# Optimization experiments

Measured on AMD Instinct MI355X. Metric: run time of the kernel, lower is better.

Reference implementation:

```python
import jax, jax.numpy as jnp
import numpy as np

VOCAB = 14
EMBED = 10
HIDDEN = 50
MLP = 50
PAD_IDX = 0
BATCH = 4096
SEQ = 2048


def setup_inputs() -> dict:
    key = jax.random.key(0)
    ks = jax.random.split(key, 10)
    tokens = jax.random.randint(ks[0], (BATCH, SEQ), 0, VOCAB, dtype=jnp.int64 if jax.config.jax_enable_x64 else jnp.int32)
    s_lstm = 1.0 / np.sqrt(HIDDEN)
    s_mlp1 = 1.0 / np.sqrt(HIDDEN)
    s_mlp2 = 1.0 / np.sqrt(MLP)
    emb = jax.random.normal(ks[1], (VOCAB, EMBED), jnp.float32)
    emb = emb.at[PAD_IDX].set(0.0)  # padding_idx row is zero in torch Embedding
    W_ih = jax.random.uniform(ks[2], (4 * HIDDEN, EMBED), jnp.float32, -s_lstm, s_lstm)
    W_hh = jax.random.uniform(ks[3], (4 * HIDDEN, HIDDEN), jnp.float32, -s_lstm, s_lstm)
    b_ih = jax.random.uniform(ks[4], (4 * HIDDEN,), jnp.float32, -s_lstm, s_lstm)
    b_hh = jax.random.uniform(ks[5], (4 * HIDDEN,), jnp.float32, -s_lstm, s_lstm)
    W1 = jax.random.uniform(ks[6], (MLP, HIDDEN), jnp.float32, -s_mlp1, s_mlp1)
    b1 = jax.random.uniform(ks[7], (MLP,), jnp.float32, -s_mlp1, s_mlp1)
    W2 = jax.random.uniform(ks[8], (1, MLP), jnp.float32, -s_mlp2, s_mlp2)
    b2 = jax.random.uniform(ks[9], (1,), jnp.float32, -s_mlp2, s_mlp2)
    return {"input": tokens, "emb": emb, "W_ih": W_ih, "W_hh": W_hh,
            "b_ih": b_ih, "b_hh": b_hh, "W1": W1, "b1": b1, "W2": W2, "b2": b2}


def reference(input, emb, W_ih, W_hh, b_ih, b_hh, W1, b1, W2, b2):
    x = emb[input]                                   # [B, T, E]
    mask = (input != PAD_IDX).astype(emb.dtype)      # [B, T]
    xs = jnp.swapaxes(x, 0, 1)                       # [T, B, E]
    ms = jnp.swapaxes(mask, 0, 1)[:, :, None]        # [T, B, 1]
    B = input.shape[0]

    def step(carry, inp):
        h, c = carry
        xt, mt = inp
        gates = xt @ W_ih.T + b_ih + h @ W_hh.T + b_hh  # [B, 4H], order i,f,g,o
        i, f, g, o = jnp.split(gates, 4, axis=-1)
        i = jax.nn.sigmoid(i)
        f = jax.nn.sigmoid(f)
        g = jnp.tanh(g)
        o = jax.nn.sigmoid(o)
        c_new = f * c + i * g
        h_new = o * jnp.tanh(c_new)
        # blend: keep old state on padded positions
        h = h_new * mt + h * (1.0 - mt)
        c = c_new * mt + c * (1.0 - mt)
        return (h, c), None

    h0 = jnp.zeros((B, HIDDEN), emb.dtype)
    c0 = jnp.zeros((B, HIDDEN), emb.dtype)
    (h, c), _ = jax.lax.scan(step, (h0, c0), (xs, ms))
    hidden = h @ W1.T + b1                            # [B, MLP]
    out = jax.nn.sigmoid(hidden @ W2.T + b2)          # [B, 1]
    return out
```

## Files before the change

kernel.cpp:

```cpp
#include <hip/hip_runtime.h>

#define BATCH 4096
#define SEQ   2048
#define EMB   10
#define HID   50
#define VOCAB 14
#define TROW  2052

using bf16x8 = __attribute__((ext_vector_type(8))) short;
using f32x4  = __attribute__((ext_vector_type(4))) float;

__device__ __forceinline__ short f2bf(float f) {
  unsigned u = __builtin_bit_cast(unsigned, f);
  u = (u + 0x7FFFu + ((u >> 16) & 1u)) >> 16;
  return (short)u;
}
__device__ __forceinline__ unsigned f2bf2(float lo, float hi) {
  return (unsigned)(unsigned short)f2bf(lo) | ((unsigned)(unsigned short)f2bf(hi) << 16);
}
__device__ __forceinline__ float fsigm(float x) {
  return __builtin_amdgcn_rcpf(1.0f + __builtin_amdgcn_exp2f(x * -1.44269504f));
}

__global__ void prep_kernel(const float* __restrict__ emb,  const float* __restrict__ W_ih,
                            const float* __restrict__ W_hh, const float* __restrict__ b_ih,
                            const float* __restrict__ b_hh, short* __restrict__ Apack) {
  int idx = blockIdx.x * 256 + threadIdx.x;
  if (idx >= 13 * 2 * 64 * 8) return;
  int j    = idx & 7;
  int lane = (idx >> 3) & 63;
  int kf   = (idx >> 9) & 1;
  int tid  = idx >> 10;
  int m    = lane & 15;
  int q    = m >> 2, g = m & 3;
  int jh   = (tid < 10) ? (2 * ((tid >> 1) * 4 + q) + (tid & 1))
                        : (40 + (tid - 10) * 4 + q);
  int k    = kf * 32 + (lane >> 4) * 8 + j;
  float v = 0.0f;
  if (jh < HID) {
    int R = g * HID + jh;
    float scale = (g == 2) ? -2.885390082f : -1.442695041f;
    if (k < HID) {
      v = W_hh[R * HID + k] * scale;
    } else {
      int vo = k - HID;
      float s = b_ih[R] + b_hh[R];
      for (int e = 0; e < EMB; ++e) s += emb[vo * EMB + e] * W_ih[R * EMB + e];
      v = s * scale;
    }
  }
  Apack[idx] = f2bf(v);
}

__global__ __launch_bounds__(512, 1) void lstm_kernel(
    const int* __restrict__ tokens, const short* __restrict__ Apack,
    const float* __restrict__ W1, const float* __restrict__ b1,
    const float* __restrict__ W2, const float* __restrict__ b2,
    float* __restrict__ out) {
  __shared__ __align__(16) unsigned char toku8[16 * TROW];
  __shared__ __align__(16) short hbuf[2][16 * 64];
  __shared__ float hfin[16 * 52];
  __shared__ float mlp_hid[16 * 52];

  const int tid  = threadIdx.x;
  const int lane = tid & 63;
  const int wv   = tid >> 6;
  const int b0   = blockIdx.x * 16;
  const int bB   = lane & 15;
  const int jj   = lane >> 4;

  const bool two = (0xA7 >> wv) & 1;
  const int  fr  = __builtin_popcount(0xA7 & ((1 << wv) - 1));
  const int  sr  = __builtin_popcount(0x58 & ((1 << wv) - 1));
  const int  p   = fr * 4 + jj;
  const int  jhS = 40 + sr * 4 + jj;
  const bool sval = !two && (jhS < HID);

  const int t0 = two ? (fr * 2) : (10 + sr);
  bf16x8 Af00 = *(const bf16x8*)(Apack + ((t0 * 2 + 0) * 64 + lane) * 8);
  bf16x8 Af01 = *(const bf16x8*)(Apack + ((t0 * 2 + 1) * 64 + lane) * 8);
  bf16x8 Af10 = {}, Af11 = {};
  if (two) {
    Af10 = *(const bf16x8*)(Apack + (((t0 + 1) * 2 + 0) * 64 + lane) * 8);
    Af11 = *(const bf16x8*)(Apack + (((t0 + 1) * 2 + 1) * 64 + lane) * 8);
  }

  const bool ohact = (wv == 3 || wv == 4) && (lane < 56);
  const int ohr   = (wv - 3) * 8 + lane / 7;
  const int ohsub = lane % 7;
  const int ohoct = (ohsub < 3) ? 6 : 7;
  const int ohinn = (ohsub < 3) ? (4 + 4 * ohsub) : (4 * (ohsub - 3));
  const int ohb   = ohr * 128 + 16 * ((ohoct + ohr) & 7) + ohinn;
  const int ohv0  = 2 * ohsub, ohv1 = 2 * ohsub + 1;

  for (int i = tid; i < 16 * 512; i += 512) {
    int row = i >> 9, c4 = i & 511;
    int4 tv = *(const int4*)&tokens[(b0 + row) * SEQ + 4 * c4];
    unsigned pk = (tv.x & 0xFF) | ((tv.y & 0xFF) << 8) |
                  ((tv.z & 0xFF) << 16) | ((tv.w & 0xFF) << 24);
    *(unsigned*)&toku8[row * TROW + 4 * c4] = pk;
  }
  for (int i = tid; i < 1024; i += 512) hbuf[0][i] = 0;
  __syncthreads();

  char* hb = (char*)hbuf;
  const int rb0   = bB * 128 + 16 * ((jj + bB) & 7);
  const int rb1   = bB * 128 + 16 * (((jj + 4) + bB) & 7);
  const int hwb32 = bB * 128 + 16 * (((p >> 2) + bB) & 7) + ((4 * p) & 15);
  const int hwb16 = bB * 128 + 16 * (((jhS >> 3) + bB) & 7) + 2 * (jhS & 7);
  const unsigned char* myrow = &toku8[bB * TROW];
  const unsigned char* ohtok = &toku8[ohr * TROW];

  if (ohact) {
    int tk = ohtok[0];
    unsigned wb = ((tk == ohv0) ? 0x3F80u : 0u) | ((tk == ohv1) ? 0x3F800000u : 0u);
    *(unsigned*)(hb + ohb) = wb;
  }

  float c0 = 0.f, h0 = 0.f, c1 = 0.f, h1 = 0.f;
  unsigned mp = 0;

  for (int t = 0; t < SEQ; t += 16) {
#pragma unroll
    for (int u = 0; u < 16; ++u) {
      const int T  = t + u;
      const int PB = (u & 1) * 2048, PN = PB ^ 2048;
      __syncthreads();

      bf16x8 Bf0 = *(const bf16x8*)(hb + PB + rb0);
      bf16x8 Bf1 = *(const bf16x8*)(hb + PB + rb1);
      if ((u & 3) == 0) mp = *(const unsigned*)(myrow + T);

      f32x4 acc0 = {0.f, 0.f, 0.f, 0.f};
      acc0 = __builtin_amdgcn_mfma_f32_16x16x32_bf16(Af00, Bf0, acc0, 0, 0, 0);
      acc0 = __builtin_amdgcn_mfma_f32_16x16x32_bf16(Af01, Bf1, acc0, 0, 0, 0);
      f32x4 acc1 = {0.f, 0.f, 0.f, 0.f};
      if (two) {
        acc1 = __builtin_amdgcn_mfma_f32_16x16x32_bf16(Af10, Bf0, acc1, 0, 0, 0);
        acc1 = __builtin_amdgcn_mfma_f32_16x16x32_bf16(Af11, Bf1, acc1, 0, 0, 0);
      }

      if (ohact && T + 1 < SEQ) {
        int tk = ohtok[T + 1];
        unsigned wb = ((tk == ohv0) ? 0x3F80u : 0u) |
                      ((tk == ohv1) ? 0x3F800000u : 0u);
        *(unsigned*)(hb + PN + ohb) = wb;
      }

      const bool keep = (((mp >> (8 * (u & 3))) & 0xFF) != 0);

      if (two) {
        float eA0 = __builtin_amdgcn_exp2f(acc0[0]);
        float eB0 = __builtin_amdgcn_exp2f(acc0[1]);
        float eC0 = __builtin_amdgcn_exp2f(acc0[2]);
        float eG0 = __builtin_amdgcn_exp2f(acc0[3]);
        float eA1 = __builtin_amdgcn_exp2f(acc1[0]);
        float eB1 = __builtin_amdgcn_exp2f(acc1[1]);
        float eC1 = __builtin_amdgcn_exp2f(acc1[2]);
        float eG1 = __builtin_amdgcn_exp2f(acc1[3]);
        float a10 = 1.f + eA0, b10 = 1.f + eB0, c10 = 1.f + eC0, g10 = 1.f + eG0;
        float a11 = 1.f + eA1, b11 = 1.f + eB1, c11 = 1.f + eC1, g11 = 1.f + eG1;
        float P0 = a10 * c10, P1 = a11 * c11;
        float t10 = __builtin_fmaf(-eC0, b10, b10);
        float t11 = __builtin_fmaf(-eC1, b11, b11);
        float num0 = __builtin_fmaf(c0, P0, t10);
        float num1 = __builtin_fmaf(c1, P1, t11);
        float den0 = P0 * b10, den1 = P1 * b11;
        float r  = __builtin_amdgcn_rcpf(den0 * den1);
        float cn0 = num0 * (den1 * r);
        float cn1 = num1 * (den0 * r);
        float cl0 = fminf(cn0 * -2.885390082f, 40.0f);
        float cl1 = fminf(cn1 * -2.885390082f, 40.0f);
        float H0 = __builtin_amdgcn_exp2f(cl0);
        float H1 = __builtin_amdgcn_exp2f(cl1);
        float hd0 = g10 * (1.f + H0);
        float hd1 = g11 * (1.f + H1);
        float rh = __builtin_amdgcn_rcpf(hd0 * hd1);
        float hn0 = (1.f - H0) * (hd1 * rh);
        float hn1 = (1.f - H1) * (hd0 * rh);
        c0 = keep ? cn0 : c0;  h0 = keep ? hn0 : h0;
        c1 = keep ? cn1 : c1;  h1 = keep ? hn1 : h1;
        *(unsigned*)(hb + PN + hwb32) = f2bf2(h0, h1);
      } else {
        float eA = __builtin_amdgcn_exp2f(acc0[0]);
        float eB = __builtin_amdgcn_exp2f(acc0[1]);
        float eC = __builtin_amdgcn_exp2f(acc0[2]);
        float eG = __builtin_amdgcn_exp2f(acc0[3]);
        float a1 = 1.f + eA, bb1 = 1.f + eB, cc1 = 1.f + eC, g1 = 1.f + eG;
        float P   = a1 * cc1;
        float t1  = __builtin_fmaf(-eC, bb1, bb1);
        float num = __builtin_fmaf(c0, P, t1);
        float den = P * bb1;
        float cn  = num * __builtin_amdgcn_rcpf(den);
        float cl  = fminf(cn * -2.885390082f, 40.0f);
        float eH  = __builtin_amdgcn_exp2f(cl);
        float hd  = g1 * (1.f + eH);
        float hn  = (1.f - eH) * __builtin_amdgcn_rcpf(hd);
        c0 = keep ? cn : c0;
        h0 = keep ? hn : h0;
        if (sval) *(short*)(hb + PN + hwb16) = f2bf(h0);
      }
    }
  }

  if (two) {
    hfin[bB * 52 + 2 * p]     = h0;
    hfin[bB * 52 + 2 * p + 1] = h1;
  } else if (sval) {
    hfin[bB * 52 + jhS] = h0;
  }
  __syncthreads();
  for (int idx = tid; idx < 16 * 64; idx += 512) {
    int b = idx >> 6, m = idx & 63;
    if (m < HID) {
      float s = b1[m];
      for (int j2 = 0; j2 < HID; ++j2) s += hfin[b * 52 + j2] * W1[m * HID + j2];
      mlp_hid[b * 52 + m] = s;
    }
  }
  __syncthreads();
  if (tid < 16) {
    float s = b2[0];
    for (int m2 = 0; m2 < HID; ++m2) s += mlp_hid[tid * 52 + m2] * W2[m2];
    out[b0 + tid] = fsigm(s);
  }
}

extern "C" void kernel_launch(void* const* d_in, const int* in_sizes, int n_in,
                              void* d_out, int out_size, void* d_ws, size_t ws_size,
                              hipStream_t stream) {
  const int*   tokens = (const int*)  d_in[0];
  const float* emb    = (const float*)d_in[1];
  const float* W_ih   = (const float*)d_in[2];
  const float* W_hh   = (const float*)d_in[3];
  const float* b_ih   = (const float*)d_in[4];
  const float* b_hh   = (const float*)d_in[5];
  const float* W1     = (const float*)d_in[6];
  const float* b1     = (const float*)d_in[7];
  const float* W2     = (const float*)d_in[8];
  const float* b2     = (const float*)d_in[9];
  float* outp  = (float*)d_out;
  short* Apack = (short*)d_ws;

  hipLaunchKernelGGL(prep_kernel, dim3(52), dim3(256), 0, stream,
                     emb, W_ih, W_hh, b_ih, b_hh, Apack);
  hipLaunchKernelGGL(lstm_kernel, dim3(BATCH / 16), dim3(512), 0, stream,
                     tokens, Apack, W1, b1, W2, b2, outp);
}
```

Baseline: 813.8 us.

## Rebalance LSTM hidden units across waves with rotating ownership of leftover units

Reassigns the 50 hidden units among the 8 waves. Four waves each own 8 units, four waves each own 4 units, and the last 2 units (48,49) are computed in rotation by one of the four thin waves per timestep. Their c/h state lives in shared memory so the rotating owner can read and update it. The goal is to even out the per-step critical path, so that no wave does two cells while another does one or none. The cost is extra LDS traffic, divergent branching and a second MFMA pair on the rotating wave, and correctness of the handoff depends on the per-step barrier ordering.

```diff
diff --git a/kernel.cpp b/kernel.cpp
--- a/kernel.cpp
+++ b/kernel.cpp
@@ -33,8 +33,10 @@
   int tid  = idx >> 10;
   int m    = lane & 15;
   int q    = m >> 2, g = m & 3;
-  int jh   = (tid < 10) ? (2 * ((tid >> 1) * 4 + q) + (tid & 1))
-                        : (40 + (tid - 10) * 4 + q);
+  int jh;
+  if (tid < 8)       { int f = tid >> 1, i = tid & 1; jh = 8 * f + 2 * q + i; }
+  else if (tid < 12) { int r = tid - 8;               jh = 32 + 4 * r + q;    }
+  else               { jh = (q < 2) ? (48 + q) : 999; }
   int k    = kf * 32 + (lane >> 4) * 8 + j;
   float v = 0.0f;
   if (jh < HID) {
@@ -59,6 +61,7 @@
     float* __restrict__ out) {
   __shared__ __align__(16) unsigned char toku8[16 * TROW];
   __shared__ __align__(16) short hbuf[2][16 * 64];
+  __shared__ float cst12[32], hst12[32];
   __shared__ float hfin[16 * 52];
   __shared__ float mlp_hid[16 * 52];
 
@@ -69,24 +72,27 @@
   const int bB   = lane & 15;
   const int jj   = lane >> 4;
 
-  const bool two = (0xA7 >> wv) & 1;
-  const int  fr  = __builtin_popcount(0xA7 & ((1 << wv) - 1));
-  const int  sr  = __builtin_popcount(0x58 & ((1 << wv) - 1));
+  const unsigned FATM = 0x96u, ROTM = 0x69u;
+  const bool fat = (FATM >> wv) & 1;
+  const int  fr  = __builtin_popcount(FATM & ((1u << wv) - 1));
+  const int  rr  = __builtin_popcount(ROTM & ((1u << wv) - 1));
   const int  p   = fr * 4 + jj;
-  const int  jhS = 40 + sr * 4 + jj;
-  const bool sval = !two && (jhS < HID);
-
-  const int t0 = two ? (fr * 2) : (10 + sr);
+  const int  jhF = 32 + 4 * rr + jj;
+
+  const int t0 = fat ? (2 * fr) : (8 + rr);
   bf16x8 Af00 = *(const bf16x8*)(Apack + ((t0 * 2 + 0) * 64 + lane) * 8);
   bf16x8 Af01 = *(const bf16x8*)(Apack + ((t0 * 2 + 1) * 64 + lane) * 8);
   bf16x8 Af10 = {}, Af11 = {};
-  if (two) {
+  if (fat) {
     Af10 = *(const bf16x8*)(Apack + (((t0 + 1) * 2 + 0) * 64 + lane) * 8);
     Af11 = *(const bf16x8*)(Apack + (((t0 + 1) * 2 + 1) * 64 + lane) * 8);
-  }
-
-  const bool ohact = (wv == 3 || wv == 4) && (lane < 56);
-  const int ohr   = (wv - 3) * 8 + lane / 7;
+  } else {
+    Af10 = *(const bf16x8*)(Apack + ((12 * 2 + 0) * 64 + lane) * 8);
+    Af11 = *(const bf16x8*)(Apack + ((12 * 2 + 1) * 64 + lane) * 8);
+  }
+
+  const bool ohact = (wv == 0 || wv == 5) && (lane < 56);
+  const int ohr   = ((wv == 5) ? 8 : 0) + lane / 7;
   const int ohsub = lane % 7;
   const int ohoct = (ohsub < 3) ? 6 : 7;
   const int ohinn = (ohsub < 3) ? (4 + 4 * ohsub) : (4 * (ohsub - 3));
@@ -101,13 +107,16 @@
     *(unsigned*)&toku8[row * TROW + 4 * c4] = pk;
   }
   for (int i = tid; i < 1024; i += 512) hbuf[0][i] = 0;
+  if (tid < 32) { cst12[tid] = 0.f; hst12[tid] = 0.f; }
   __syncthreads();
 
   char* hb = (char*)hbuf;
   const int rb0   = bB * 128 + 16 * ((jj + bB) & 7);
   const int rb1   = bB * 128 + 16 * (((jj + 4) + bB) & 7);
   const int hwb32 = bB * 128 + 16 * (((p >> 2) + bB) & 7) + ((4 * p) & 15);
-  const int hwb16 = bB * 128 + 16 * (((jhS >> 3) + bB) & 7) + 2 * (jhS & 7);
+  const int hwb16 = bB * 128 + 16 * (((jhF >> 3) + bB) & 7) + 2 * (jhF & 7);
+  const int hw12  = bB * 128 + 16 * ((6 + bB) & 7) + 2 * jj;
+  const int ci    = jj * 16 + bB;
   const unsigned char* myrow = &toku8[bB * TROW];
   const unsigned char* ohtok = &toku8[ohr * TROW];
 
@@ -129,16 +138,6 @@
 
       bf16x8 Bf0 = *(const bf16x8*)(hb + PB + rb0);
       bf16x8 Bf1 = *(const bf16x8*)(hb + PB + rb1);
-      if ((u & 3) == 0) mp = *(const unsigned*)(myrow + T);
-
-      f32x4 acc0 = {0.f, 0.f, 0.f, 0.f};
-      acc0 = __builtin_amdgcn_mfma_f32_16x16x32_bf16(Af00, Bf0, acc0, 0, 0, 0);
-      acc0 = __builtin_amdgcn_mfma_f32_16x16x32_bf16(Af01, Bf1, acc0, 0, 0, 0);
-      f32x4 acc1 = {0.f, 0.f, 0.f, 0.f};
-      if (two) {
-        acc1 = __builtin_amdgcn_mfma_f32_16x16x32_bf16(Af10, Bf0, acc1, 0, 0, 0);
-        acc1 = __builtin_amdgcn_mfma_f32_16x16x32_bf16(Af11, Bf1, acc1, 0, 0, 0);
-      }
 
       if (ohact && T + 1 < SEQ) {
         int tk = ohtok[T + 1];
@@ -146,41 +145,66 @@
                       ((tk == ohv1) ? 0x3F800000u : 0u);
         *(unsigned*)(hb + PN + ohb) = wb;
       }
+      if ((u & 3) == 0) mp = *(const unsigned*)(myrow + T);
+
+      f32x4 acc0 = {0.f, 0.f, 0.f, 0.f};
+      acc0 = __builtin_amdgcn_mfma_f32_16x16x32_bf16(Af00, Bf0, acc0, 0, 0, 0);
+      acc0 = __builtin_amdgcn_mfma_f32_16x16x32_bf16(Af01, Bf1, acc0, 0, 0, 0);
 
       const bool keep = (((mp >> (8 * (u & 3))) & 0xFF) != 0);
 
-      if (two) {
-        float eA0 = __builtin_amdgcn_exp2f(acc0[0]);
-        float eB0 = __builtin_amdgcn_exp2f(acc0[1]);
-        float eC0 = __builtin_amdgcn_exp2f(acc0[2]);
-        float eG0 = __builtin_amdgcn_exp2f(acc0[3]);
-        float eA1 = __builtin_amdgcn_exp2f(acc1[0]);
-        float eB1 = __builtin_amdgcn_exp2f(acc1[1]);
-        float eC1 = __builtin_amdgcn_exp2f(acc1[2]);
-        float eG1 = __builtin_amdgcn_exp2f(acc1[3]);
-        float a10 = 1.f + eA0, b10 = 1.f + eB0, c10 = 1.f + eC0, g10 = 1.f + eG0;
-        float a11 = 1.f + eA1, b11 = 1.f + eB1, c11 = 1.f + eC1, g11 = 1.f + eG1;
-        float P0 = a10 * c10, P1 = a11 * c11;
-        float t10 = __builtin_fmaf(-eC0, b10, b10);
-        float t11 = __builtin_fmaf(-eC1, b11, b11);
-        float num0 = __builtin_fmaf(c0, P0, t10);
-        float num1 = __builtin_fmaf(c1, P1, t11);
-        float den0 = P0 * b10, den1 = P1 * b11;
-        float r  = __builtin_amdgcn_rcpf(den0 * den1);
-        float cn0 = num0 * (den1 * r);
-        float cn1 = num1 * (den0 * r);
-        float cl0 = fminf(cn0 * -2.885390082f, 40.0f);
-        float cl1 = fminf(cn1 * -2.885390082f, 40.0f);
-        float H0 = __builtin_amdgcn_exp2f(cl0);
-        float H1 = __builtin_amdgcn_exp2f(cl1);
-        float hd0 = g10 * (1.f + H0);
-        float hd1 = g11 * (1.f + H1);
-        float rh = __builtin_amdgcn_rcpf(hd0 * hd1);
-        float hn0 = (1.f - H0) * (hd1 * rh);
-        float hn1 = (1.f - H1) * (hd0 * rh);
-        c0 = keep ? cn0 : c0;  h0 = keep ? hn0 : h0;
-        c1 = keep ? cn1 : c1;  h1 = keep ? hn1 : h1;
+#define CELL2(ACCA, ACCB, CA, HA, CB, HB)                                      \
+      {                                                                        \
+        float eA0 = __builtin_amdgcn_exp2f(ACCA[0]);                           \
+        float eB0 = __builtin_amdgcn_exp2f(ACCA[1]);                           \
+        float eC0 = __builtin_amdgcn_exp2f(ACCA[2]);                           \
+        float eG0 = __builtin_amdgcn_exp2f(ACCA[3]);                           \
+        float eA1 = __builtin_amdgcn_exp2f(ACCB[0]);                           \
+        float eB1 = __builtin_amdgcn_exp2f(ACCB[1]);                           \
+        float eC1 = __builtin_amdgcn_exp2f(ACCB[2]);                           \
+        float eG1 = __builtin_amdgcn_exp2f(ACCB[3]);                           \
+        float a10 = 1.f + eA0, b10 = 1.f + eB0, c10 = 1.f + eC0, g10 = 1.f + eG0; \
+        float a11 = 1.f + eA1, b11 = 1.f + eB1, c11 = 1.f + eC1, g11 = 1.f + eG1; \
+        float P0 = a10 * c10, P1 = a11 * c11;                                  \
+        float t10 = __builtin_fmaf(-eC0, b10, b10);                            \
+        float t11 = __builtin_fmaf(-eC1, b11, b11);                            \
+        float num0 = __builtin_fmaf(CA, P0, t10);                              \
+        float num1 = __builtin_fmaf(CB, P1, t11);                              \
+        float den0 = P0 * b10, den1 = P1 * b11;                                \
+        float r  = __builtin_amdgcn_rcpf(den0 * den1);                         \
+        float cn0 = num0 * (den1 * r);                                         \
+        float cn1 = num1 * (den0 * r);                                         \
+        float cl0 = fminf(cn0 * -2.885390082f, 40.0f);                         \
+        float cl1 = fminf(cn1 * -2.885390082f, 40.0f);                         \
+        float H0 = __builtin_amdgcn_exp2f(cl0);                                \
+        float H1 = __builtin_amdgcn_exp2f(cl1);                                \
+        float hd0 = g10 * (1.f + H0);                                          \
+        float hd1 = g11 * (1.f + H1);                                          \
+        float rh = __builtin_amdgcn_rcpf(hd0 * hd1);                           \
+        float hn0 = (1.f - H0) * (hd1 * rh);                                   \
+        float hn1 = (1.f - H1) * (hd0 * rh);                                   \
+        CA = keep ? cn0 : CA;  HA = keep ? hn0 : HA;                           \
+        CB = keep ? cn1 : CB;  HB = keep ? hn1 : HB;                           \
+      }
+
+      if (fat) {
+        f32x4 acc1 = {0.f, 0.f, 0.f, 0.f};
+        acc1 = __builtin_amdgcn_mfma_f32_16x16x32_bf16(Af10, Bf0, acc1, 0, 0, 0);
+        acc1 = __builtin_amdgcn_mfma_f32_16x16x32_bf16(Af11, Bf1, acc1, 0, 0, 0);
+        CELL2(acc0, acc1, c0, h0, c1, h1)
         *(unsigned*)(hb + PN + hwb32) = f2bf2(h0, h1);
+      } else if ((T & 3) == rr) {
+        f32x4 acc2 = {0.f, 0.f, 0.f, 0.f};
+        acc2 = __builtin_amdgcn_mfma_f32_16x16x32_bf16(Af10, Bf0, acc2, 0, 0, 0);
+        acc2 = __builtin_amdgcn_mfma_f32_16x16x32_bf16(Af11, Bf1, acc2, 0, 0, 0);
+        float cO = 0.f, hO = 0.f;
+        if (jj < 2) { cO = cst12[ci]; hO = hst12[ci]; }
+        CELL2(acc0, acc2, c0, h0, cO, hO)
+        *(short*)(hb + PN + hwb16) = f2bf(h0);
+        if (jj < 2) {
+          cst12[ci] = cO; hst12[ci] = hO;
+          *(short*)(hb + PN + hw12) = f2bf(hO);
+        }
       } else {
         float eA = __builtin_amdgcn_exp2f(acc0[0]);
         float eB = __builtin_amdgcn_exp2f(acc0[1]);
@@ -198,17 +222,20 @@
         float hn  = (1.f - eH) * __builtin_amdgcn_rcpf(hd);
         c0 = keep ? cn : c0;
         h0 = keep ? hn : h0;
-        if (sval) *(short*)(hb + PN + hwb16) = f2bf(h0);
+        *(short*)(hb + PN + hwb16) = f2bf(h0);
       }
+#undef CELL2
     }
   }
 
-  if (two) {
+  if (fat) {
     hfin[bB * 52 + 2 * p]     = h0;
     hfin[bB * 52 + 2 * p + 1] = h1;
-  } else if (sval) {
-    hfin[bB * 52 + jhS] = h0;
-  }
+  } else {
+    hfin[bB * 52 + jhF] = h0;
+  }
+  __syncthreads();
+  if (wv == 0 && jj < 2) hfin[bB * 52 + 48 + jj] = hst12[ci];
   __syncthreads();
   for (int idx = tid; idx < 16 * 64; idx += 512) {
     int b = idx >> 6, m = idx & 63;
```

Result: slower. 909.3 us (+11.7%).
